# Kernel tuning notes

Hardware: AMD Instinct MI355X
Metric: run time of the kernel (lower is better)

The kernel has to match this reference:

```python
import jax, jax.numpy as jnp
import numpy as np

NQ, N, C = 8192, 32768, 128


def setup_inputs() -> dict:
    key = jax.random.key(0)
    k1, k2, k3 = jax.random.split(key, 3)
    return {
        "query_pos": jax.random.normal(k1, (NQ, 3), dtype=jnp.float32),
        "neural_feat": jax.random.normal(k2, (N, C), dtype=jnp.float32),
        "neural_pos": jax.random.normal(k3, (N, 3), dtype=jnp.float32),
        "knn": 64,
    }


def _cdist(a, b):
    # Euclidean pairwise distances via the (|a|^2 + |b|^2 - 2ab) expansion.
    a2 = jnp.sum(a * a, axis=-1, keepdims=True)          # [N',1]
    b2 = jnp.sum(b * b, axis=-1)                          # [N]
    d2 = a2 + b2[None, :] - 2.0 * (a @ b.T)               # [N',N]
    return jnp.sqrt(jnp.maximum(d2, 1e-12))


def reference(query_pos, neural_feat, neural_pos, knn):
    dists = _cdist(query_pos, neural_pos)                 # [N',N]
    # torch.topk(largest=False, sorted=True) == top_k of negated dists.
    neg_vals, closest_ind = jax.lax.top_k(-dists, knn)    # [N',k]
    closest_dists = -neg_vals                             # ascending
    closest_feat = neural_feat[closest_ind]               # [N',k,C] gather
    inv_dist = 1.0 / (closest_dists + 1e-5)               # [N',k]
    retrieved_feat = jnp.sum(closest_feat * inv_dist[..., None], axis=1)  # [N',C]
    return retrieved_feat
```

## Files before the change

kernel.cpp:

```cpp
#include <hip/hip_runtime.h>
#include <math.h>

#define NQ    8192
#define NPTS  32768
#define KNN   64
#define CAP   256
#define PG    64
#define PNC   (PG*PG*PG)
#define PCELL 0.15f
#define PGINV (PG / 9.6f)
#define QG    32
#define QNC   (QG*QG*QG)
#define QGINV (QG / 9.6f)
#define GLO   (-4.8f)
#define NBLK  2048
#define TGT   (110.0f / 32768.0f)
#define PCHUNKS (PNC / 1024)
#define QCHUNKS (QNC / 1024)

__device__ __forceinline__ unsigned key_of(float f) {
  unsigned u = __float_as_uint(f);
  return (u & 0x80000000u) ? ~u : (u | 0x80000000u);
}
__device__ __forceinline__ float val_of(unsigned k) {
  unsigned u = (k & 0x80000000u) ? (k & 0x7fffffffu) : ~k;
  return __uint_as_float(u);
}
__device__ __forceinline__ int mbcnt64(unsigned long long m) {
  return __builtin_amdgcn_mbcnt_hi((unsigned)(m >> 32),
         __builtin_amdgcn_mbcnt_lo((unsigned)m, 0));
}
__device__ __forceinline__ float rflf(float x) {
  return __int_as_float(__builtin_amdgcn_readfirstlane(__float_as_int(x)));
}
__device__ __forceinline__ int rfli(int x) { return __builtin_amdgcn_readfirstlane(x); }

__device__ __forceinline__ float norm_cdf(float x) { return 0.5f * erfcf(-x * 0.70710678f); }
__device__ __forceinline__ float ball_mass(float mu, float r) {
  float a = r - mu, b = r + mu;
  float e = __expf(-0.5f * b * b) - __expf(-0.5f * a * a);
  return e / (mu * 2.50662827f) + norm_cdf(a) - norm_cdf(-mu) + norm_cdf(b) - norm_cdf(mu);
}

__device__ __forceinline__ int cidxP(float v) {
  int i = (int)floorf((v - GLO) * PGINV);
  return min(max(i, 0), PG - 1);
}
__device__ __forceinline__ int cidxQ(float v) {
  int i = (int)floorf((v - GLO) * QGINV);
  return min(max(i, 0), QG - 1);
}


__global__ __launch_bounds__(256) void hist_tau_kernel(
    const float* __restrict__ pos, const float* __restrict__ qpos,
    int* __restrict__ pcnt, int* __restrict__ qcnt, float* __restrict__ tau) {
  const int gid = blockIdx.x * 256 + threadIdx.x;
  const float x = pos[gid * 3 + 0], y = pos[gid * 3 + 1], z = pos[gid * 3 + 2];
  atomicAdd(&pcnt[(cidxP(z) * PG + cidxP(y)) * PG + cidxP(x)], 1);
  if (gid < NQ) {
    const float qx = qpos[gid * 3 + 0], qy = qpos[gid * 3 + 1], qz = qpos[gid * 3 + 2];
    atomicAdd(&qcnt[(cidxQ(qz) * QG + cidxQ(qy)) * QG + cidxQ(qx)], 1);
    const float b = qx * qx + qy * qy + qz * qz;
    const float mu = fmaxf(sqrtf(b), 0.05f);
    float lo = 0.f, hi = mu + 8.f;
    for (int i = 0; i < 16; ++i) {
      const float r = 0.5f * (lo + hi);
      if (ball_mass(mu, r) < TGT) lo = r; else hi = r;
    }
    tau[gid] = hi * hi;
  }
}

__global__ __launch_bounds__(256) void scan_kernel(
    int* __restrict__ pcnt, int* __restrict__ qcnt, int* __restrict__ cellStart,
    int* __restrict__ ppub, int* __restrict__ qpub) {
  __shared__ int aux[256];
  __shared__ int off[256];
  const int t = threadIdx.x;
  const bool isP = (blockIdx.x < PCHUNKS);
  const int cb = isP ? blockIdx.x : (blockIdx.x - PCHUNKS);
  int* src = isP ? pcnt : qcnt;
  int* pub = isP ? ppub : qpub;
  const int base = cb * 1024 + t * 4;
  const int4 q = ((const int4*)(src + base))[0];
  aux[t] = q.x + q.y + q.z + q.w;
  __syncthreads();
  for (int o = 1; o < 256; o <<= 1) {
    const int u = (t >= o) ? aux[t - o] : 0;
    __syncthreads();
    aux[t] += u;
    __syncthreads();
  }
  if (t == 0) atomicExch(&pub[cb], aux[255] + 1);
  int v = 0;
  if (t < cb) {
    while ((v = atomicOr(&pub[t], 0)) == 0) { }
    v -= 1;
  }
  off[t] = v;
  __syncthreads();
  for (int o = 128; o; o >>= 1) {
    if (t < o) off[t] += off[t + o];
    __syncthreads();
  }
  const int chunkOff = off[0];
  int run = (t ? aux[t - 1] : 0) + chunkOff;
  int4 w;
  w.x = run; run += q.x;
  w.y = run; run += q.y;
  w.z = run; run += q.z;
  w.w = run; run += q.w;
  if (isP) {
    ((int4*)(cellStart + base))[0] = w;
    ((int4*)(pcnt + base))[0] = w;
    if (cb == PCHUNKS - 1 && t == 255) cellStart[PNC] = NPTS;
  } else {
    ((int4*)(qcnt + base))[0] = w;
  }
}

__global__ __launch_bounds__(256) void scatter_kernel(
    const float* __restrict__ pos, const float* __restrict__ qpos,
    int* __restrict__ pcur, int* __restrict__ qcur, const float* __restrict__ tau,
    float4* __restrict__ pts, float4* __restrict__ qp, float* __restrict__ qtau) {
  const int gid = blockIdx.x * 256 + threadIdx.x;
  const float x = pos[gid * 3 + 0], y = pos[gid * 3 + 1], z = pos[gid * 3 + 2];
  const int c = (cidxP(z) * PG + cidxP(y)) * PG + cidxP(x);
  const int slot = atomicAdd(&pcur[c], 1);
  pts[slot] = make_float4(x, y, z, __int_as_float(gid));
  if (gid < NQ) {
    const float a = qpos[gid * 3 + 0], b = qpos[gid * 3 + 1], d = qpos[gid * 3 + 2];
    const int qc = (cidxQ(d) * QG + cidxQ(b)) * QG + cidxQ(a);
    const int qs = atomicAdd(&qcur[qc], 1);
    qp[qs] = make_float4(a, b, d, __int_as_float(gid));
    qtau[qs] = tau[gid];
  }
}


__global__ __launch_bounds__(256, 8) void knn_main(
    const float* __restrict__ feat, const int* __restrict__ cellStart,
    const float4* __restrict__ pts, const float4* __restrict__ qp,
    const float* __restrict__ qtau, float* __restrict__ out) {

  __shared__ uint2 sCand[4][CAP];
  __shared__ uint2 sSel[4][KNN];

  const int tid = threadIdx.x, lane = tid & 63, wv = tid >> 6;
  const int bid = blockIdx.x;
  const int swz = (bid & 7) * (NBLK / 8) + (bid >> 3);
  const int sq  = swz * 4 + wv;

  const float4 Q = qp[sq];
  const float qx = rflf(Q.x), qy = rflf(Q.y), qz = rflf(Q.z);
  const int orig = rfli(__float_as_int(Q.w));
  const float bq = qx * qx + qy * qy + qz * qz;
  const float nx = -2.f * qx, ny = -2.f * qy, nz = -2.f * qz;
  float r2 = rflf(qtau[sq]);
  float tlo = 0.f, thi = -1.f;
  int cnt = 0;

  for (int attempt = 0; attempt < 12; ++attempt) {
    const float r = sqrtf(r2);
    const float tq = r2 - bq;
    const int iy0 = cidxP(qy - r), iy1 = cidxP(qy + r);
    const int iz0 = cidxP(qz - r), iz1 = cidxP(qz + r);
    const int nyw  = iy1 - iy0 + 1;
    const int nrow = nyw * (iz1 - iz0 + 1);
    cnt = 0;
    for (int rc = 0; rc < nrow; rc += 64) {
      const int myrow = rc + lane;
      int s = 0, c = 0;
      if (myrow < nrow) {
        const int dz = myrow / nyw;
        const int dy = myrow - dz * nyw;
        const int giy = iy0 + dy, giz = iz0 + dz;
        const float ylo = GLO + giy * PCELL;
        const float zlo = GLO + giz * PCELL;
        const float dyv = fmaxf(0.f, fmaxf(ylo - qy, qy - (ylo + PCELL)));
        const float dzv = fmaxf(0.f, fmaxf(zlo - qz, qz - (zlo + PCELL)));
        const float dd = dyv * dyv + dzv * dzv;
        if (dd < r2) {
          const float hx = sqrtf(r2 - dd);
          const int jx0 = cidxP(qx - hx), jx1 = cidxP(qx + hx);
          const int rb = (giz * PG + giy) * PG;
          s = cellStart[rb + jx0];
          c = cellStart[rb + jx1 + 1] - s;
        }
      }
      int cum = c;
      #pragma unroll
      for (int off = 1; off < 64; off <<= 1) {
        const int u = __shfl_up(cum, off);
        if (lane >= off) cum += u;
      }
      const int adj = s - (cum - c);
      const int Tc = __shfl(cum, 63);
      for (int b = 0; b < Tc; b += 64) {
        const int fi = b + lane;
        const bool have = fi < Tc;
        int ro = 0;
        #pragma unroll
        for (int st = 32; st; st >>= 1) {
          const int nr = ro + st;
          const int probe = __shfl(cum, min(nr, 64) - 1);
          if (nr <= 64 && probe <= fi) ro = nr;
        }
        const int pi = fi + __shfl(adj, min(ro, 63));
        const float4 P = pts[have ? pi : 0];
        const float n = P.x * P.x + P.y * P.y + P.z * P.z;
        const float d = fmaf(P.z, nz, fmaf(P.y, ny, fmaf(P.x, nx, n)));
        const bool hh = have && (d < tq);
        const unsigned long long m = __ballot(hh);
        if (m) {
          const int p = cnt + mbcnt64(m);
          if (hh && p < CAP)
            sCand[wv][p] = make_uint2(key_of(d + bq), __float_as_uint(P.w));
          cnt += (int)__popcll(m);
        }
      }
    }
    if (cnt >= KNN && cnt <= CAP) break;
    if (cnt < KNN) { tlo = r2; r2 = (thi < 0.f) ? r2 * 3.f : 0.5f * (r2 + thi); }
    else           { thi = r2; r2 = 0.5f * (tlo + r2); }
  }

  {
    const int mm = min(cnt, CAP);
    unsigned k[4], id[4];
    #pragma unroll
    for (int s = 0; s < 4; ++s) {
      const int g2 = s * 64 + lane;
      uint2 kv = make_uint2(0xFFFFFFFFu, 0u);
      if (g2 < mm) kv = sCand[wv][g2];
      k[s] = kv.x; id[s] = kv.y;
    }
    unsigned blo = 0x80000000u, bhi = 0xFFFFFFFFu;
    for (int it = 0; it < 32; ++it) {
      const unsigned mid = blo + ((bhi - blo) >> 1);
      const int c = (int)(__popcll(__ballot(k[0] <= mid)) + __popcll(__ballot(k[1] <= mid)) +
                          __popcll(__ballot(k[2] <= mid)) + __popcll(__ballot(k[3] <= mid)));
      if (c >= KNN) bhi = mid; else blo = mid + 1;
    }
    const unsigned K = blo;

    int fill = 0;
    #pragma unroll
    for (int s = 0; s < 4; ++s) {
      const bool lt = k[s] < K;
      const unsigned long long msk = __ballot(lt);
      if (msk) {
        const int p = fill + mbcnt64(msk);
        if (lt) { const float dv = val_of(k[s]);
                  const float w_ = 1.f / (sqrtf(fmaxf(dv, 1e-12f)) + 1e-5f);
                  sSel[wv][p] = make_uint2(id[s], __float_as_uint(w_)); }
        fill += (int)__popcll(msk);
      }
    }
    #pragma unroll
    for (int s = 0; s < 4; ++s) {
      const bool eq = (k[s] == K);
      const unsigned long long msk = __ballot(eq);
      if (msk) {
        const int p = fill + mbcnt64(msk);
        if (eq && p < KNN) { const float dv = val_of(k[s]);
                             const float w_ = 1.f / (sqrtf(fmaxf(dv, 1e-12f)) + 1e-5f);
                             sSel[wv][p] = make_uint2(id[s], __float_as_uint(w_)); }
        fill += (int)__popcll(msk);
      }
    }
  }

  {
    const int half = lane >> 5;
    const int col  = lane & 31;
    float4 acc = make_float4(0.f, 0.f, 0.f, 0.f);
    #pragma unroll 4
    for (int j = 0; j < KNN; j += 2) {
      const uint2 pr = sSel[wv][j + half];
      const float w = __uint_as_float(pr.y);
      const float4 f4 = *(const float4*)(feat + ((size_t)pr.x << 7) + (col << 2));
      acc.x = fmaf(w, f4.x, acc.x);
      acc.y = fmaf(w, f4.y, acc.y);
      acc.z = fmaf(w, f4.z, acc.z);
      acc.w = fmaf(w, f4.w, acc.w);
    }
    acc.x += __shfl_xor(acc.x, 32);
    acc.y += __shfl_xor(acc.y, 32);
    acc.z += __shfl_xor(acc.z, 32);
    acc.w += __shfl_xor(acc.w, 32);
    if (lane < 32)
      *(float4*)(out + ((size_t)orig << 7) + (col << 2)) = acc;
  }
}

extern "C" void kernel_launch(void* const* d_in, const int* in_sizes, int n_in,
                              void* d_out, int out_size, void* d_ws, size_t ws_size,
                              hipStream_t stream) {
  const float* qpos = (const float*)d_in[0];
  const float* feat = (const float*)d_in[1];
  const float* pos  = (const float*)d_in[2];
  float* out = (float*)d_out;

  char* ws = (char*)d_ws;
  int*    pcnt      = (int*)(ws);
  int*    qcnt      = (int*)(ws + (1024 << 10));
  int*    ppub      = (int*)(ws + (1152 << 10));
  int*    qpub      = (int*)(ws + (1153 << 10));
  int*    cellStart = (int*)(ws + (1156 << 10));
  float*  tau       = (float*)(ws + (2188 << 10));
  float4* pts       = (float4*)(ws + (2220 << 10));
  float4* qp        = (float4*)(ws + (2732 << 10));
  float*  qtau      = (float*)(ws + (2860 << 10));

  hipMemsetAsync(ws, 0, 1154 << 10, stream);
  hist_tau_kernel<<<dim3(NPTS / 256),        dim3(256), 0, stream>>>(pos, qpos, pcnt, qcnt, tau);
  scan_kernel    <<<dim3(PCHUNKS + QCHUNKS), dim3(256), 0, stream>>>(pcnt, qcnt, cellStart, ppub, qpub);
  scatter_kernel <<<dim3(NPTS / 256),        dim3(256), 0, stream>>>(pos, qpos, pcnt, qcnt, tau, pts, qp, qtau);
  knn_main       <<<dim3(NBLK),              dim3(256), 0, stream>>>(feat, cellStart, pts, qp, qtau, out);
}
```

Baseline: 118.4 us.

## Batch cell-row ranges in LDS across row chunks and prefetch next chunk's cellStart

Instead of scanning candidate points per 64-row chunk (leaving lanes idle when a chunk holds few points), nonempty row ranges are accumulated into per-wave LDS buffers across chunks and drained together. This packs point probes densely into full 64-lane batches. The cellStart loads for the next row chunk are also issued ahead of processing the current one. The cost is extra LDS (about 8KB per block), which may lower occupancy, plus a binary search in LDS when more than 64 ranges are buffered.

```diff
diff --git a/kernel.cpp b/kernel.cpp
--- a/kernel.cpp
+++ b/kernel.cpp
@@ -5,6 +5,7 @@
 #define NPTS  32768
 #define KNN   64
 #define CAP   256
+#define RCAP  256
 #define PG    64
 #define PNC   (PG*PG*PG)
 #define PCELL 0.15f
@@ -146,6 +147,8 @@
 
   __shared__ uint2 sCand[4][CAP];
   __shared__ uint2 sSel[4][KNN];
+  __shared__ int   sRC[4][RCAP];
+  __shared__ int   sAdj[4][RCAP];
 
   const int tid = threadIdx.x, lane = tid & 63, wv = tid >> 6;
   const int bid = blockIdx.x;
@@ -169,9 +172,60 @@
     const int nyw  = iy1 - iy0 + 1;
     const int nrow = nyw * (iz1 - iz0 + 1);
     cnt = 0;
-    for (int rc = 0; rc < nrow; rc += 64) {
-      const int myrow = rc + lane;
-      int s = 0, c = 0;
+    int nbuf = 0, tot = 0;
+
+    auto probe_pt = [&](int pi, bool have) {
+      const float4 P = pts[have ? pi : 0];
+      const float n = P.x * P.x + P.y * P.y + P.z * P.z;
+      const float d = fmaf(P.z, nz, fmaf(P.y, ny, fmaf(P.x, nx, n)));
+      const bool hh = have && (d < tq);
+      const unsigned long long m = __ballot(hh);
+      if (m) {
+        const int p = cnt + mbcnt64(m);
+        if (hh && p < CAP)
+          sCand[wv][p] = make_uint2(key_of(d + bq), __float_as_uint(P.w));
+        cnt += (int)__popcll(m);
+      }
+    };
+
+    auto drain = [&]() {
+      if (nbuf == 0) return;
+      if (nbuf <= 64) {
+        const int rcv = (lane < nbuf) ? sRC[wv][lane] : 0x7FFFFFFF;
+        const int adv = (lane < nbuf) ? sAdj[wv][lane] : 0;
+        for (int b = 0; b < tot; b += 64) {
+          const int fi = b + lane;
+          const bool have = fi < tot;
+          int ro = 0;
+          #pragma unroll
+          for (int st = 32; st; st >>= 1) {
+            const int nr = ro + st;
+            const int probe = __shfl(rcv, min(nr, nbuf) - 1);
+            if (nr <= nbuf && probe <= fi) ro = nr;
+          }
+          const int pi = fi + __shfl(adv, min(ro, nbuf - 1));
+          probe_pt(pi, have);
+        }
+      } else {
+        for (int b = 0; b < tot; b += 64) {
+          const int fi = b + lane;
+          const bool have = fi < tot;
+          int ro = 0;
+          #pragma unroll
+          for (int st = 128; st; st >>= 1) {
+            const int nr = ro + st;
+            if (nr <= nbuf && sRC[wv][nr - 1] <= fi) ro = nr;
+          }
+          const int pi = fi + sAdj[wv][min(ro, nbuf - 1)];
+          probe_pt(pi, have);
+        }
+      }
+      nbuf = 0; tot = 0;
+    };
+
+    auto issue = [&](int rcb, int& sR, int& eR, bool& vd) {
+      vd = false; sR = 0; eR = 0;
+      const int myrow = rcb + lane;
       if (myrow < nrow) {
         const int dz = myrow / nyw;
         const int dy = myrow - dz * nyw;
@@ -185,42 +239,39 @@
           const float hx = sqrtf(r2 - dd);
           const int jx0 = cidxP(qx - hx), jx1 = cidxP(qx + hx);
           const int rb = (giz * PG + giy) * PG;
-          s = cellStart[rb + jx0];
-          c = cellStart[rb + jx1 + 1] - s;
+          sR = cellStart[rb + jx0];
+          eR = cellStart[rb + jx1 + 1];
+          vd = true;
         }
       }
+    };
+
+    int sR0 = 0, eR0 = 0; bool v0 = false;
+    issue(0, sR0, eR0, v0);
+    for (int rc = 0; rc < nrow; rc += 64) {
+      int sR1 = 0, eR1 = 0; bool v1 = false;
+      if (rc + 64 < nrow) issue(rc + 64, sR1, eR1, v1);
+      const int c = v0 ? (eR0 - sR0) : 0;
+      const int s = v0 ? sR0 : 0;
       int cum = c;
       #pragma unroll
       for (int off = 1; off < 64; off <<= 1) {
         const int u = __shfl_up(cum, off);
         if (lane >= off) cum += u;
       }
-      const int adj = s - (cum - c);
-      const int Tc = __shfl(cum, 63);
-      for (int b = 0; b < Tc; b += 64) {
-        const int fi = b + lane;
-        const bool have = fi < Tc;
-        int ro = 0;
-        #pragma unroll
-        for (int st = 32; st; st >>= 1) {
-          const int nr = ro + st;
-          const int probe = __shfl(cum, min(nr, 64) - 1);
-          if (nr <= 64 && probe <= fi) ro = nr;
-        }
-        const int pi = fi + __shfl(adj, min(ro, 63));
-        const float4 P = pts[have ? pi : 0];
-        const float n = P.x * P.x + P.y * P.y + P.z * P.z;
-        const float d = fmaf(P.z, nz, fmaf(P.y, ny, fmaf(P.x, nx, n)));
-        const bool hh = have && (d < tq);
-        const unsigned long long m = __ballot(hh);
-        if (m) {
-          const int p = cnt + mbcnt64(m);
-          if (hh && p < CAP)
-            sCand[wv][p] = make_uint2(key_of(d + bq), __float_as_uint(P.w));
-          cnt += (int)__popcll(m);
-        }
-      }
-    }
+      const unsigned long long act = __ballot(c > 0);
+      const int slot = nbuf + mbcnt64(act);
+      if (c > 0) {
+        sRC[wv][slot]  = tot + cum;
+        sAdj[wv][slot] = s - (tot + cum - c);
+      }
+      nbuf += (int)__popcll(act);
+      tot  += __shfl(cum, 63);
+      if (nbuf > RCAP - 64) drain();
+      sR0 = sR1; eR0 = eR1; v0 = v1;
+    }
+    drain();
+
     if (cnt >= KNN && cnt <= CAP) break;
     if (cnt < KNN) { tlo = r2; r2 = (thi < 0.f) ? r2 * 3.f : 0.5f * (r2 + thi); }
     else           { thi = r2; r2 = 0.5f * (tlo + r2); }
```

Result: faster. 116.0 us (median of 2 runs) (-2.1%).
